# Kernel tuning notes

Measured on AMD Instinct MI355X. Metric: run time of the kernel, lower is better.

The kernel has to match this reference:

```python
import jax, jax.numpy as jnp
import numpy as np

N = 100000      # nodes
E = 1600000     # directed edges
F_IN = 9        # atom features (fixed by GCNConv(9, hidden))
H = 128         # hidden_channels
G = 64          # graphs in batch


def setup_inputs() -> dict:
    key = jax.random.key(0)
    ks = jax.random.split(key, 12)
    x = jax.random.normal(ks[0], (N, F_IN), dtype=jnp.float32)
    edge_index = jax.random.randint(ks[1], (2, E), 0, N, dtype=jnp.int64)
    batch = jnp.sort(jax.random.randint(ks[2], (N,), 0, G, dtype=jnp.int64))
    def lin_init(k, fan_in, fan_out):
        s = 1.0 / np.sqrt(fan_in)
        kw, kb = jax.random.split(k)
        W = jax.random.uniform(kw, (fan_in, fan_out), jnp.float32, -s, s)
        b = jax.random.uniform(kb, (fan_out,), jnp.float32, -s, s)
        return W, b
    W1, b1 = lin_init(ks[3], F_IN, H)
    W2, b2 = lin_init(ks[4], H, H)
    W3, b3 = lin_init(ks[5], H, H)
    lin_w, lin_b = lin_init(ks[6], H, 1)
    return {"x": x, "edge_index": edge_index, "batch": batch,
            "W1": W1, "b1": b1, "W2": W2, "b2": b2, "W3": W3, "b3": b3,
            "lin_w": lin_w, "lin_b": lin_b}


def reference(x, edge_index, batch, W1, b1, W2, b2, W3, b3, lin_w, lin_b):
    n = x.shape[0]
    # PyG GCNConv default: add self-loops, symmetric normalization D^-1/2 (A+I) D^-1/2
    loops = jnp.arange(n, dtype=edge_index.dtype)
    src = jnp.concatenate([edge_index[0], loops])   # [E+N]
    dst = jnp.concatenate([edge_index[1], loops])   # [E+N]
    deg = jax.ops.segment_sum(jnp.ones_like(dst, dtype=x.dtype), dst, num_segments=n)
    dinv = jnp.where(deg > 0, jax.lax.rsqrt(jnp.maximum(deg, 1e-12)), 0.0)
    norm = (dinv[src] * dinv[dst])[:, None]         # [E+N, 1]

    def gcn_conv(h, W, b):
        hw = h @ W                                   # [N, H]
        msg = hw[src] * norm                         # gather + scale  [E+N, H]
        return jax.ops.segment_sum(msg, dst, num_segments=n) + b  # scatter-add

    h = jax.nn.relu(gcn_conv(x, W1, b1))
    h = jax.nn.relu(gcn_conv(h, W2, b2))
    h = gcn_conv(h, W3, b3)

    # global_mean_pool over graph ids
    counts = jax.ops.segment_sum(jnp.ones((n,), x.dtype), batch, num_segments=G)
    pooled = jax.ops.segment_sum(h, batch, num_segments=G) / jnp.maximum(counts, 1.0)[:, None]
    return pooled @ lin_w + lin_b                    # [G, 1]
```

## Files before the change

kernel.cpp:

```cpp
#include <hip/hip_runtime.h>
#include <math.h>


#define CHUNK 2048

__device__ __forceinline__ int rankof(int i, int nq, int nr) {
  int c = i & 7;
  return c * nq + min(c, nr) + (i >> 3);
}
__device__ __forceinline__ unsigned short f2bf(float f) {
  unsigned int u = __float_as_uint(f);
  return (unsigned short)((u + 0x7fff + ((u >> 16) & 1)) >> 16);
}
__device__ __forceinline__ float bflo(unsigned int u) { return __uint_as_float(u << 16); }
__device__ __forceinline__ float bfhi(unsigned int u) { return __uint_as_float(u & 0xffff0000u); }


__global__ void deg_kernel(const int* __restrict__ dst, int* cnt_rank,
                           int E, int nq, int nr) {
  int e = blockIdx.x * blockDim.x + threadIdx.x;
  if (e < E) atomicAdd(&cnt_rank[rankof(dst[e], nq, nr)], 1);
}

__global__ void dinv_bsum_pad_kernel(const int* __restrict__ cnt_rank,
                                     float* __restrict__ dinv, int* bsum,
                                     const float* __restrict__ x,
                                     float* __restrict__ xp, int N, int nq, int nr) {
  __shared__ int s[256];
  int t = threadIdx.x;
  int gid = blockIdx.x * 256 + t;
  s[t] = (gid < N) ? cnt_rank[gid] : 0;
  if (gid < N) {
    int c = cnt_rank[rankof(gid, nq, nr)];
    float di = 1.0f / sqrtf((float)c + 1.0f);
    dinv[gid] = di;
    const float* xr = x + (size_t)gid * 9;
    float* xo = xp + (size_t)gid * 16;
    *(float4*)(xo + 0)  = make_float4(xr[0] * di, xr[1] * di, xr[2] * di, xr[3] * di);
    *(float4*)(xo + 4)  = make_float4(xr[4] * di, xr[5] * di, xr[6] * di, xr[7] * di);
    *(float4*)(xo + 8)  = make_float4(xr[8] * di, 0.0f, 0.0f, 0.0f);
    *(float4*)(xo + 12) = make_float4(0.0f, 0.0f, 0.0f, 0.0f);
  }
  __syncthreads();
  for (int off = 128; off > 0; off >>= 1) {
    if (t < off) s[t] += s[t + off];
    __syncthreads();
  }
  if (t == 0) bsum[blockIdx.x] = s[0];
}

__global__ void rowptr_vc0_kernel(const int* __restrict__ indeg, const int* __restrict__ bsum,
                                  int2* __restrict__ rows, int* cursor, int N, int E,
                                  int nq, int nr,
                                  const float* __restrict__ W3, const float* __restrict__ b3,
                                  const float* __restrict__ lin_w, const float* __restrict__ lin_b,
                                  float* v, float* c0) {
  __shared__ int ps[256];
  __shared__ int s[256];
  int t = threadIdx.x;
  int pref = 0;
  for (int q = t; q < blockIdx.x; q += 256) pref += bsum[q];
  ps[t] = pref;
  __syncthreads();
  for (int off = 128; off > 0; off >>= 1) {
    if (t < off) ps[t] += ps[t + off];
    __syncthreads();
  }
  int base = ps[0];
  int r = blockIdx.x * 256 + t;
  int val = (r < N) ? indeg[r] : 0;
  s[t] = val;
  __syncthreads();
  for (int off = 1; off < 256; off <<= 1) {
    int x = (t >= off) ? s[t - off] : 0;
    __syncthreads();
    s[t] += x;
    __syncthreads();
  }
  int excl = s[t] - val + base;
  if (r < N) {
    cursor[r] = excl;
    int c = 0;
#pragma unroll
    for (int cc = 1; cc < 8; ++cc) {
      int b = cc * nq + min(cc, nr);
      if (r >= b) c = cc;
    }
    int iinv = ((r - (c * nq + min(c, nr))) << 3) | c;
    rows[iinv] = make_int2(excl, excl + val);
  }
  if (blockIdx.x == 0) {
    if (t < 128) {
      float sv = 0.0f;
      for (int c = 0; c < 128; ++c) sv = fmaf(W3[t * 128 + c], lin_w[c], sv);
      v[t] = sv;
    } else if (t == 128) {
      float sv = 0.0f;
      for (int c = 0; c < 128; ++c) sv = fmaf(b3[c], lin_w[c], sv);
      c0[0] = sv + lin_b[0];
    }
  }
}

__global__ __launch_bounds__(256) void fill_part_kernel(const int* __restrict__ src,
                                                        const int* __restrict__ dst,
                                                        int* cursor, int* __restrict__ col,
                                                        int E, int nq, int nr) {
  int sub = blockIdx.x & 7;
  int base = (blockIdx.x >> 3) * CHUNK;
#pragma unroll
  for (int j = 0; j < CHUNK / 256; ++j) {
    int e = base + j * 256 + threadIdx.x;
    if (e < E) {
      int d = dst[e];
      if ((d & 7) == sub) {
        int p = atomicAdd(&cursor[rankof(d, nq, nr)], 1);
        col[p] = src[e];
      }
    }
  }
}


__global__ __launch_bounds__(256) void agg9_gemm1_kernel(const float* __restrict__ xp,
    const float* __restrict__ dinv, const int2* __restrict__ rows,
    const int* __restrict__ col, const float* __restrict__ W1,
    const float* __restrict__ b1, unsigned short* __restrict__ hA, int N) {
  __shared__ float sW[9 * 128];
  __shared__ float sx[256 * 9];
  __shared__ float sdi[256];
  int tid = threadIdx.x;
  for (int q = tid; q < 9 * 128; q += 256) sW[q] = W1[q];
  int i = blockIdx.x * 256 + tid;
  float4 A0, A1, A2, B0, B1, B2;
  A0 = A1 = A2 = B0 = B1 = B2 = make_float4(0.f, 0.f, 0.f, 0.f);
  float di = 0.0f;
  if (i < N) {
    di = dinv[i];
    const float4* xi = (const float4*)(xp + (size_t)i * 16);
    A0 = xi[0]; A1 = xi[1]; A2 = xi[2];
    int2 rw = rows[i];
    int rs = rw.x, re = rw.y;
    int e = rs;
    for (; e + 2 <= re; e += 2) {
      int c0 = __builtin_nontemporal_load(&col[e]);
      int c1 = __builtin_nontemporal_load(&col[e + 1]);
      const float4* q0 = (const float4*)(xp + (size_t)c0 * 16);
      const float4* q1 = (const float4*)(xp + (size_t)c1 * 16);
      float4 r0 = q0[0], r1 = q0[1], r2 = q0[2];
      float4 u0 = q1[0], u1 = q1[1], u2 = q1[2];
      A0.x += r0.x; A0.y += r0.y; A0.z += r0.z; A0.w += r0.w;
      A1.x += r1.x; A1.y += r1.y; A1.z += r1.z; A1.w += r1.w;
      A2.x += r2.x;
      B0.x += u0.x; B0.y += u0.y; B0.z += u0.z; B0.w += u0.w;
      B1.x += u1.x; B1.y += u1.y; B1.z += u1.z; B1.w += u1.w;
      B2.x += u2.x;
    }
    if (e < re) {
      int c0 = __builtin_nontemporal_load(&col[e]);
      const float4* q0 = (const float4*)(xp + (size_t)c0 * 16);
      float4 r0 = q0[0], r1 = q0[1], r2 = q0[2];
      A0.x += r0.x; A0.y += r0.y; A0.z += r0.z; A0.w += r0.w;
      A1.x += r1.x; A1.y += r1.y; A1.z += r1.z; A1.w += r1.w;
      A2.x += r2.x;
    }
  }
  sdi[tid] = di;
  float* so = sx + tid * 9;
  so[0] = (A0.x + B0.x) * di; so[1] = (A0.y + B0.y) * di; so[2] = (A0.z + B0.z) * di;
  so[3] = (A0.w + B0.w) * di; so[4] = (A1.x + B1.x) * di; so[5] = (A1.y + B1.y) * di;
  so[6] = (A1.z + B1.z) * di; so[7] = (A1.w + B1.w) * di; so[8] = (A2.x + B2.x) * di;
  __syncthreads();
  int c2 = tid & 63, rsub = tid >> 6;
  float wA[9], wB[9];
#pragma unroll
  for (int f = 0; f < 9; ++f) {
    wA[f] = sW[f * 128 + 2 * c2];
    wB[f] = sW[f * 128 + 2 * c2 + 1];
  }
  float biasA = b1[2 * c2], biasB = b1[2 * c2 + 1];
  int base = blockIdx.x * 256;
  for (int j = 0; j < 64; ++j) {
    int rl = j * 4 + rsub;
    int row = base + rl;
    if (row >= N) break;
    float sA = biasA, sB = biasB;
#pragma unroll
    for (int f = 0; f < 9; ++f) {
      float xv = sx[rl * 9 + f];
      sA = fmaf(xv, wA[f], sA);
      sB = fmaf(xv, wB[f], sB);
    }
    float d = sdi[rl];
    unsigned int pk = (unsigned int)f2bf(fmaxf(sA, 0.0f) * d)
                    | ((unsigned int)f2bf(fmaxf(sB, 0.0f) * d) << 16);
    *(unsigned int*)(hA + (size_t)row * 128 + 2 * c2) = pk;
  }
}


__global__ __launch_bounds__(256) void aggH_kernel(const unsigned short* __restrict__ h,
    const int2* __restrict__ rows, const int* __restrict__ col,
    float* __restrict__ g, int N) {
  int wave = threadIdx.x >> 6;
  int lane = threadIdx.x & 63;
  int half = lane >> 5;
  int l32  = lane & 31;
  int i = blockIdx.x * 4 + wave;
  if (i >= N) return;
  uint2 sp = *((const uint2*)(h + (size_t)i * 128) + l32);
  float m = half ? 0.0f : 1.0f;
  float4 a0 = make_float4(bflo(sp.x) * m, bfhi(sp.x) * m, bflo(sp.y) * m, bfhi(sp.y) * m);
  float4 a1 = make_float4(0.f, 0.f, 0.f, 0.f);
  float4 a2 = make_float4(0.f, 0.f, 0.f, 0.f);
  float4 a3 = make_float4(0.f, 0.f, 0.f, 0.f);
  int2 rw = rows[i];
  int rs = rw.x, re = rw.y;
  int e = rs;
  for (; e + 8 <= re; e += 8) {
    int c0 = __builtin_nontemporal_load(&col[e + half]);
    int c1 = __builtin_nontemporal_load(&col[e + 2 + half]);
    int c2 = __builtin_nontemporal_load(&col[e + 4 + half]);
    int c3 = __builtin_nontemporal_load(&col[e + 6 + half]);
    uint2 p0 = *((const uint2*)(h + (size_t)c0 * 128) + l32);
    uint2 p1 = *((const uint2*)(h + (size_t)c1 * 128) + l32);
    uint2 p2 = *((const uint2*)(h + (size_t)c2 * 128) + l32);
    uint2 p3 = *((const uint2*)(h + (size_t)c3 * 128) + l32);
    a0.x += bflo(p0.x); a0.y += bfhi(p0.x); a0.z += bflo(p0.y); a0.w += bfhi(p0.y);
    a1.x += bflo(p1.x); a1.y += bfhi(p1.x); a1.z += bflo(p1.y); a1.w += bfhi(p1.y);
    a2.x += bflo(p2.x); a2.y += bfhi(p2.x); a2.z += bflo(p2.y); a2.w += bfhi(p2.y);
    a3.x += bflo(p3.x); a3.y += bfhi(p3.x); a3.z += bflo(p3.y); a3.w += bfhi(p3.y);
  }
  if (e + 4 <= re) {
    int c0 = __builtin_nontemporal_load(&col[e + half]);
    int c1 = __builtin_nontemporal_load(&col[e + 2 + half]);
    uint2 p0 = *((const uint2*)(h + (size_t)c0 * 128) + l32);
    uint2 p1 = *((const uint2*)(h + (size_t)c1 * 128) + l32);
    a0.x += bflo(p0.x); a0.y += bfhi(p0.x); a0.z += bflo(p0.y); a0.w += bfhi(p0.y);
    a1.x += bflo(p1.x); a1.y += bfhi(p1.x); a1.z += bflo(p1.y); a1.w += bfhi(p1.y);
    e += 4;
  }
  if (e + 2 <= re) {
    int c0 = __builtin_nontemporal_load(&col[e + half]);
    uint2 p0 = *((const uint2*)(h + (size_t)c0 * 128) + l32);
    a2.x += bflo(p0.x); a2.y += bfhi(p0.x); a2.z += bflo(p0.y); a2.w += bfhi(p0.y);
    e += 2;
  }
  if (e < re) {
    int c0 = __builtin_nontemporal_load(&col[e]);
    uint2 p0 = *((const uint2*)(h + (size_t)c0 * 128) + l32);
    a3.x = fmaf(bflo(p0.x), 0.5f, a3.x); a3.y = fmaf(bfhi(p0.x), 0.5f, a3.y);
    a3.z = fmaf(bflo(p0.y), 0.5f, a3.z); a3.w = fmaf(bfhi(p0.y), 0.5f, a3.w);
  }
  float4 a = make_float4((a0.x + a1.x) + (a2.x + a3.x), (a0.y + a1.y) + (a2.y + a3.y),
                         (a0.z + a1.z) + (a2.z + a3.z), (a0.w + a1.w) + (a2.w + a3.w));
  a.x += __shfl_down(a.x, 32, 64);
  a.y += __shfl_down(a.y, 32, 64);
  a.z += __shfl_down(a.z, 32, 64);
  a.w += __shfl_down(a.w, 32, 64);
  if (half == 0) *((float4*)(g + (size_t)i * 128) + l32) = a;
}


__global__ __launch_bounds__(256, 4) void gemmz_kernel(const float* __restrict__ g,
    const float* __restrict__ W2, const float* __restrict__ dinv,
    const float* __restrict__ b2, const float* __restrict__ v,
    float* __restrict__ zd, int N) {
  __shared__ float Hs[32 * 132];
  __shared__ float Ws[32 * 128];
  int tid = threadIdx.x;
  int rb = blockIdx.x * 128;
  int tr = tid >> 4, tc = tid & 15;
  float acc[8][8];
#pragma unroll
  for (int r = 0; r < 8; ++r)
#pragma unroll
    for (int c = 0; c < 8; ++c) acc[r][c] = 0.0f;

  for (int kc = 0; kc < 128; kc += 32) {
#pragma unroll
    for (int j = 0; j < 4; ++j) {
      int q = tid + j * 256;
      int row = q >> 3;
      int kk = (q & 7) * 4;
      float4 vv = make_float4(0.f, 0.f, 0.f, 0.f);
      int grow = rb + row;
      if (grow < N) vv = *(const float4*)&g[(size_t)grow * 128 + kc + kk];
      Hs[(kk + 0) * 132 + row] = vv.x;
      Hs[(kk + 1) * 132 + row] = vv.y;
      Hs[(kk + 2) * 132 + row] = vv.z;
      Hs[(kk + 3) * 132 + row] = vv.w;
    }
#pragma unroll
    for (int j = 0; j < 4; ++j) {
      int q = tid + j * 256;
      int kr = q >> 5;
      int c4 = (q & 31) * 4;
      *(float4*)&Ws[kr * 128 + c4] = *(const float4*)&W2[(size_t)(kc + kr) * 128 + c4];
    }
    __syncthreads();
#pragma unroll 4
    for (int kk = 0; kk < 32; ++kk) {
      float4 h0 = *(const float4*)&Hs[kk * 132 + tr * 8];
      float4 h1 = *(const float4*)&Hs[kk * 132 + tr * 8 + 4];
      float4 w0 = *(const float4*)&Ws[kk * 128 + tc * 8];
      float4 w1 = *(const float4*)&Ws[kk * 128 + tc * 8 + 4];
      float av[8] = {h0.x, h0.y, h0.z, h0.w, h1.x, h1.y, h1.z, h1.w};
      float bv[8] = {w0.x, w0.y, w0.z, w0.w, w1.x, w1.y, w1.z, w1.w};
#pragma unroll
      for (int r = 0; r < 8; ++r)
#pragma unroll
        for (int c = 0; c < 8; ++c) acc[r][c] = fmaf(av[r], bv[c], acc[r][c]);
    }
    __syncthreads();
  }
  float4 ba = *((const float4*)b2 + tc * 2);
  float4 bb = *((const float4*)b2 + tc * 2 + 1);
  float4 va = *((const float4*)v + tc * 2);
  float4 vb = *((const float4*)v + tc * 2 + 1);
  float bc[8] = {ba.x, ba.y, ba.z, ba.w, bb.x, bb.y, bb.z, bb.w};
  float vc[8] = {va.x, va.y, va.z, va.w, vb.x, vb.y, vb.z, vb.w};
  float* red = Ws;
#pragma unroll
  for (int r = 0; r < 8; ++r) {
    int row = rb + tr * 8 + r;
    float p = 0.0f;
    if (row < N) {
      float dr = dinv[row];
#pragma unroll
      for (int c = 0; c < 8; ++c)
        p += fmaxf(fmaf(dr, acc[r][c], bc[c]), 0.0f) * vc[c];
    }
    red[(tr * 8 + r) * 17 + tc] = p;
  }
  __syncthreads();
  if (tid < 128) {
    int row = rb + tid;
    if (row < N) {
      float s = 0.0f;
#pragma unroll
      for (int j = 0; j < 16; ++j) s += red[tid * 17 + j];
      zd[row] = dinv[row] * s;
    }
  }
}


__global__ void agg1_pool_kernel(const float* __restrict__ zd, const float* __restrict__ dinv,
    const int2* __restrict__ rows, const int* __restrict__ col,
    const int* __restrict__ batch, float* gsum, float* gcnt, int N) {
  __shared__ float lsum[64];
  __shared__ float lcnt[64];
  int t = threadIdx.x;
  if (t < 64) { lsum[t] = 0.0f; lcnt[t] = 0.0f; }
  __syncthreads();
  int i = blockIdx.x * blockDim.x + t;
  if (i < N) {
    float acc = zd[i];
    int2 rw = rows[i];
    int rs = rw.x, re = rw.y;
    int e = rs;
    for (; e + 4 <= re; e += 4) {
      float z0 = zd[col[e]], z1 = zd[col[e + 1]];
      float z2 = zd[col[e + 2]], z3 = zd[col[e + 3]];
      acc += (z0 + z1) + (z2 + z3);
    }
    for (; e < re; ++e) acc += zd[col[e]];
    acc *= dinv[i];
    int gidx = batch[i];
    atomicAdd(&lsum[gidx], acc);
    atomicAdd(&lcnt[gidx], 1.0f);
  }
  __syncthreads();
  if (t < 64) {
    if (lsum[t] != 0.0f) atomicAdd(&gsum[t], lsum[t]);
    if (lcnt[t] != 0.0f) atomicAdd(&gcnt[t], lcnt[t]);
  }
}

__global__ void final_kernel(const float* __restrict__ gsum, const float* __restrict__ gcnt,
                             const float* __restrict__ c0, float* out, int G) {
  int g = threadIdx.x;
  if (g < G) out[g] = gsum[g] / fmaxf(gcnt[g], 1.0f) + c0[0];
}


extern "C" void kernel_launch(void* const* d_in, const int* in_sizes, int n_in,
                              void* d_out, int out_size, void* d_ws, size_t ws_size,
                              hipStream_t stream) {
  const float* x      = (const float*)d_in[0];
  const int*   eidx   = (const int*)d_in[1];
  const int*   batch  = (const int*)d_in[2];
  const float* W1     = (const float*)d_in[3];
  const float* b1     = (const float*)d_in[4];
  const float* W2     = (const float*)d_in[5];
  const float* b2     = (const float*)d_in[6];
  const float* W3     = (const float*)d_in[7];
  const float* b3     = (const float*)d_in[8];
  const float* lin_w  = (const float*)d_in[9];
  const float* lin_b  = (const float*)d_in[10];
  float* out = (float*)d_out;

  int N = in_sizes[0] / 9;
  int E = in_sizes[1] / 2;
  int G = out_size;
  const int* src = eidx;
  const int* dst = eidx + E;
  int nq = N >> 3, nr = N & 7;

  char* w = (char*)d_ws;
  size_t off = 0;
  auto alloc = [&](size_t bytes) -> void* {
    void* p = w + off;
    off += bytes;
    off = (off + 255) & ~(size_t)255;
    return p;
  };

  int nb = (N + 255) / 256;
  int nchunk = (E + CHUNK - 1) / CHUNK;
  int*   cursor = (int*)  alloc((size_t)N * 4);
  float* gsum   = (float*)alloc(64 * 4);
  float* gcnt   = (float*)alloc(64 * 4);
  size_t zspan = off;
  float* dinv   = (float*)alloc((size_t)N * 4);
  int2*  rows   = (int2*) alloc((size_t)N * 8);
  int*   bsum   = (int*)  alloc((size_t)nb * 4);
  int*   colsrc = (int*)  alloc((size_t)E * 4);
  unsigned short* hA = (unsigned short*)alloc((size_t)N * 128 * 2);
  float* g      = (float*)alloc((size_t)N * 128 * 4);
  float* zd     = (float*)alloc((size_t)N * 4);
  float* v      = (float*)alloc(128 * 4);
  float* c0     = (float*)alloc(4);
  float* xp     = g;

  hipMemsetAsync(d_ws, 0, zspan, stream);
  deg_kernel<<<(E + 255) / 256, 256, 0, stream>>>(dst, cursor, E, nq, nr);
  dinv_bsum_pad_kernel<<<nb, 256, 0, stream>>>(cursor, dinv, bsum, x, xp, N, nq, nr);
  rowptr_vc0_kernel<<<nb, 256, 0, stream>>>(cursor, bsum, rows, cursor, N, E, nq, nr,
                                            W3, b3, lin_w, lin_b, v, c0);
  fill_part_kernel<<<nchunk * 8, 256, 0, stream>>>(src, dst, cursor, colsrc, E, nq, nr);
  agg9_gemm1_kernel<<<nb, 256, 0, stream>>>(xp, dinv, rows, colsrc, W1, b1, hA, N);
  aggH_kernel<<<(N + 3) / 4, 256, 0, stream>>>(hA, rows, colsrc, g, N);
  gemmz_kernel<<<(N + 127) / 128, 256, 0, stream>>>(g, W2, dinv, b2, v, zd, N);
  agg1_pool_kernel<<<nb, 256, 0, stream>>>(zd, dinv, rows, colsrc, batch, gsum, gcnt, N);
  final_kernel<<<1, 64, 0, stream>>>(gsum, gcnt, c0, out, G);
}
```

Measured before the change: 409.8 us.

## Store aggregated hidden features in bf16 and widen aggH gathers to 16-byte loads

The layer-2 aggregation output g is now stored as packed bf16 instead of fp32, and the GEMM loader unpacks it. This halves the write traffic in aggH and the read traffic in gemmz. aggH also switches to 16-byte loads, with quarter-wave lanes covering four edges at a time, and uses a masked tail plus an xor-shuffle reduction. The first-layer aggregation loop is unrolled by 4. Rounding the aggregated features to bf16 adds some precision loss before the GEMM.

```diff
diff --git a/kernel.cpp b/kernel.cpp
--- a/kernel.cpp
+++ b/kernel.cpp
@@ -8,12 +8,22 @@
   int c = i & 7;
   return c * nq + min(c, nr) + (i >> 3);
 }
-__device__ __forceinline__ unsigned short f2bf(float f) {
+__device__ __forceinline__ unsigned int f2bf(float f) {
   unsigned int u = __float_as_uint(f);
-  return (unsigned short)((u + 0x7fff + ((u >> 16) & 1)) >> 16);
+  return ((u + 0x7fff + ((u >> 16) & 1)) >> 16);
 }
 __device__ __forceinline__ float bflo(unsigned int u) { return __uint_as_float(u << 16); }
 __device__ __forceinline__ float bfhi(unsigned int u) { return __uint_as_float(u & 0xffff0000u); }
+__device__ __forceinline__ void acc8(float4& p, float4& q, uint4 v) {
+  p.x += bflo(v.x); p.y += bfhi(v.x); p.z += bflo(v.y); p.w += bfhi(v.y);
+  q.x += bflo(v.z); q.y += bfhi(v.z); q.z += bflo(v.w); q.w += bfhi(v.w);
+}
+__device__ __forceinline__ void acc8w(float4& p, float4& q, uint4 v, float w) {
+  p.x = fmaf(bflo(v.x), w, p.x); p.y = fmaf(bfhi(v.x), w, p.y);
+  p.z = fmaf(bflo(v.y), w, p.z); p.w = fmaf(bfhi(v.y), w, p.w);
+  q.x = fmaf(bflo(v.z), w, q.x); q.y = fmaf(bfhi(v.z), w, q.y);
+  q.z = fmaf(bflo(v.w), w, q.z); q.w = fmaf(bfhi(v.w), w, q.w);
+}
 
 
 __global__ void deg_kernel(const int* __restrict__ dst, int* cnt_rank,
@@ -142,6 +152,32 @@
     int2 rw = rows[i];
     int rs = rw.x, re = rw.y;
     int e = rs;
+    for (; e + 4 <= re; e += 4) {
+      int c0 = __builtin_nontemporal_load(&col[e]);
+      int c1 = __builtin_nontemporal_load(&col[e + 1]);
+      int c2 = __builtin_nontemporal_load(&col[e + 2]);
+      int c3 = __builtin_nontemporal_load(&col[e + 3]);
+      const float4* q0 = (const float4*)(xp + (size_t)c0 * 16);
+      const float4* q1 = (const float4*)(xp + (size_t)c1 * 16);
+      const float4* q2 = (const float4*)(xp + (size_t)c2 * 16);
+      const float4* q3 = (const float4*)(xp + (size_t)c3 * 16);
+      float4 r0 = q0[0], r1 = q0[1], r2 = q0[2];
+      float4 u0 = q1[0], u1 = q1[1], u2 = q1[2];
+      float4 v0 = q2[0], v1 = q2[1], v2 = q2[2];
+      float4 w0 = q3[0], w1 = q3[1], w2 = q3[2];
+      A0.x += r0.x; A0.y += r0.y; A0.z += r0.z; A0.w += r0.w;
+      A1.x += r1.x; A1.y += r1.y; A1.z += r1.z; A1.w += r1.w;
+      A2.x += r2.x;
+      B0.x += u0.x; B0.y += u0.y; B0.z += u0.z; B0.w += u0.w;
+      B1.x += u1.x; B1.y += u1.y; B1.z += u1.z; B1.w += u1.w;
+      B2.x += u2.x;
+      A0.x += v0.x; A0.y += v0.y; A0.z += v0.z; A0.w += v0.w;
+      A1.x += v1.x; A1.y += v1.y; A1.z += v1.z; A1.w += v1.w;
+      A2.x += v2.x;
+      B0.x += w0.x; B0.y += w0.y; B0.z += w0.z; B0.w += w0.w;
+      B1.x += w1.x; B1.y += w1.y; B1.z += w1.z; B1.w += w1.w;
+      B2.x += w2.x;
+    }
     for (; e + 2 <= re; e += 2) {
       int c0 = __builtin_nontemporal_load(&col[e]);
       int c1 = __builtin_nontemporal_load(&col[e + 1]);
@@ -171,14 +207,14 @@
   so[3] = (A0.w + B0.w) * di; so[4] = (A1.x + B1.x) * di; so[5] = (A1.y + B1.y) * di;
   so[6] = (A1.z + B1.z) * di; so[7] = (A1.w + B1.w) * di; so[8] = (A2.x + B2.x) * di;
   __syncthreads();
-  int c2 = tid & 63, rsub = tid >> 6;
+  int c2i = tid & 63, rsub = tid >> 6;
   float wA[9], wB[9];
 #pragma unroll
   for (int f = 0; f < 9; ++f) {
-    wA[f] = sW[f * 128 + 2 * c2];
-    wB[f] = sW[f * 128 + 2 * c2 + 1];
-  }
-  float biasA = b1[2 * c2], biasB = b1[2 * c2 + 1];
+    wA[f] = sW[f * 128 + 2 * c2i];
+    wB[f] = sW[f * 128 + 2 * c2i + 1];
+  }
+  float biasA = b1[2 * c2i], biasB = b1[2 * c2i + 1];
   int base = blockIdx.x * 256;
   for (int j = 0; j < 64; ++j) {
     int rl = j * 4 + rsub;
@@ -192,77 +228,75 @@
       sB = fmaf(xv, wB[f], sB);
     }
     float d = sdi[rl];
-    unsigned int pk = (unsigned int)f2bf(fmaxf(sA, 0.0f) * d)
-                    | ((unsigned int)f2bf(fmaxf(sB, 0.0f) * d) << 16);
-    *(unsigned int*)(hA + (size_t)row * 128 + 2 * c2) = pk;
+    unsigned int pk = f2bf(fmaxf(sA, 0.0f) * d) | (f2bf(fmaxf(sB, 0.0f) * d) << 16);
+    *(unsigned int*)(hA + (size_t)row * 128 + 2 * c2i) = pk;
   }
 }
 
 
 __global__ __launch_bounds__(256) void aggH_kernel(const unsigned short* __restrict__ h,
     const int2* __restrict__ rows, const int* __restrict__ col,
-    float* __restrict__ g, int N) {
+    unsigned short* __restrict__ g, int N) {
   int wave = threadIdx.x >> 6;
   int lane = threadIdx.x & 63;
-  int half = lane >> 5;
-  int l32  = lane & 31;
+  int q4 = lane >> 4;
+  int l16 = lane & 15;
   int i = blockIdx.x * 4 + wave;
   if (i >= N) return;
-  uint2 sp = *((const uint2*)(h + (size_t)i * 128) + l32);
-  float m = half ? 0.0f : 1.0f;
-  float4 a0 = make_float4(bflo(sp.x) * m, bfhi(sp.x) * m, bflo(sp.y) * m, bfhi(sp.y) * m);
-  float4 a1 = make_float4(0.f, 0.f, 0.f, 0.f);
-  float4 a2 = make_float4(0.f, 0.f, 0.f, 0.f);
-  float4 a3 = make_float4(0.f, 0.f, 0.f, 0.f);
+  uint4 sp = *((const uint4*)(h + (size_t)i * 128) + l16);
+  float m = (q4 == 0) ? 1.0f : 0.0f;
+  float4 A0 = make_float4(0.f, 0.f, 0.f, 0.f), A1 = A0, B0 = A0, B1 = A0;
+  float4 C0 = A0, C1 = A0, D0 = A0, D1 = A0;
+  acc8w(A0, A1, sp, m);
   int2 rw = rows[i];
   int rs = rw.x, re = rw.y;
   int e = rs;
-  for (; e + 8 <= re; e += 8) {
-    int c0 = __builtin_nontemporal_load(&col[e + half]);
-    int c1 = __builtin_nontemporal_load(&col[e + 2 + half]);
-    int c2 = __builtin_nontemporal_load(&col[e + 4 + half]);
-    int c3 = __builtin_nontemporal_load(&col[e + 6 + half]);
-    uint2 p0 = *((const uint2*)(h + (size_t)c0 * 128) + l32);
-    uint2 p1 = *((const uint2*)(h + (size_t)c1 * 128) + l32);
-    uint2 p2 = *((const uint2*)(h + (size_t)c2 * 128) + l32);
-    uint2 p3 = *((const uint2*)(h + (size_t)c3 * 128) + l32);
-    a0.x += bflo(p0.x); a0.y += bfhi(p0.x); a0.z += bflo(p0.y); a0.w += bfhi(p0.y);
-    a1.x += bflo(p1.x); a1.y += bfhi(p1.x); a1.z += bflo(p1.y); a1.w += bfhi(p1.y);
-    a2.x += bflo(p2.x); a2.y += bfhi(p2.x); a2.z += bflo(p2.y); a2.w += bfhi(p2.y);
-    a3.x += bflo(p3.x); a3.y += bfhi(p3.x); a3.z += bflo(p3.y); a3.w += bfhi(p3.y);
-  }
-  if (e + 4 <= re) {
-    int c0 = __builtin_nontemporal_load(&col[e + half]);
-    int c1 = __builtin_nontemporal_load(&col[e + 2 + half]);
-    uint2 p0 = *((const uint2*)(h + (size_t)c0 * 128) + l32);
-    uint2 p1 = *((const uint2*)(h + (size_t)c1 * 128) + l32);
-    a0.x += bflo(p0.x); a0.y += bfhi(p0.x); a0.z += bflo(p0.y); a0.w += bfhi(p0.y);
-    a1.x += bflo(p1.x); a1.y += bfhi(p1.x); a1.z += bflo(p1.y); a1.w += bfhi(p1.y);
-    e += 4;
-  }
-  if (e + 2 <= re) {
-    int c0 = __builtin_nontemporal_load(&col[e + half]);
-    uint2 p0 = *((const uint2*)(h + (size_t)c0 * 128) + l32);
-    a2.x += bflo(p0.x); a2.y += bfhi(p0.x); a2.z += bflo(p0.y); a2.w += bfhi(p0.y);
-    e += 2;
+  for (; e + 16 <= re; e += 16) {
+    int c0 = __builtin_nontemporal_load(&col[e + q4]);
+    int c1 = __builtin_nontemporal_load(&col[e + 4 + q4]);
+    int c2 = __builtin_nontemporal_load(&col[e + 8 + q4]);
+    int c3 = __builtin_nontemporal_load(&col[e + 12 + q4]);
+    uint4 p0 = *((const uint4*)(h + (size_t)c0 * 128) + l16);
+    uint4 p1 = *((const uint4*)(h + (size_t)c1 * 128) + l16);
+    uint4 p2 = *((const uint4*)(h + (size_t)c2 * 128) + l16);
+    uint4 p3 = *((const uint4*)(h + (size_t)c3 * 128) + l16);
+    acc8(A0, A1, p0); acc8(B0, B1, p1); acc8(C0, C1, p2); acc8(D0, D1, p3);
+  }
+  for (; e + 4 <= re; e += 4) {
+    int c0 = __builtin_nontemporal_load(&col[e + q4]);
+    uint4 p0 = *((const uint4*)(h + (size_t)c0 * 128) + l16);
+    acc8(C0, C1, p0);
   }
   if (e < re) {
-    int c0 = __builtin_nontemporal_load(&col[e]);
-    uint2 p0 = *((const uint2*)(h + (size_t)c0 * 128) + l32);
-    a3.x = fmaf(bflo(p0.x), 0.5f, a3.x); a3.y = fmaf(bfhi(p0.x), 0.5f, a3.y);
-    a3.z = fmaf(bflo(p0.y), 0.5f, a3.z); a3.w = fmaf(bfhi(p0.y), 0.5f, a3.w);
-  }
-  float4 a = make_float4((a0.x + a1.x) + (a2.x + a3.x), (a0.y + a1.y) + (a2.y + a3.y),
-                         (a0.z + a1.z) + (a2.z + a3.z), (a0.w + a1.w) + (a2.w + a3.w));
-  a.x += __shfl_down(a.x, 32, 64);
-  a.y += __shfl_down(a.y, 32, 64);
-  a.z += __shfl_down(a.z, 32, 64);
-  a.w += __shfl_down(a.w, 32, 64);
-  if (half == 0) *((float4*)(g + (size_t)i * 128) + l32) = a;
-}
-
-
-__global__ __launch_bounds__(256, 4) void gemmz_kernel(const float* __restrict__ g,
+    int idx = e + q4;
+    int c0 = __builtin_nontemporal_load(&col[min(idx, re - 1)]);
+    uint4 p0 = *((const uint4*)(h + (size_t)c0 * 128) + l16);
+    float w = (idx < re) ? 1.0f : 0.0f;
+    acc8w(D0, D1, p0, w);
+  }
+  float4 s0 = make_float4((A0.x + B0.x) + (C0.x + D0.x), (A0.y + B0.y) + (C0.y + D0.y),
+                          (A0.z + B0.z) + (C0.z + D0.z), (A0.w + B0.w) + (C0.w + D0.w));
+  float4 s1 = make_float4((A1.x + B1.x) + (C1.x + D1.x), (A1.y + B1.y) + (C1.y + D1.y),
+                          (A1.z + B1.z) + (C1.z + D1.z), (A1.w + B1.w) + (C1.w + D1.w));
+#pragma unroll
+  for (int mk = 16; mk <= 32; mk <<= 1) {
+    s0.x += __shfl_xor(s0.x, mk, 64); s0.y += __shfl_xor(s0.y, mk, 64);
+    s0.z += __shfl_xor(s0.z, mk, 64); s0.w += __shfl_xor(s0.w, mk, 64);
+    s1.x += __shfl_xor(s1.x, mk, 64); s1.y += __shfl_xor(s1.y, mk, 64);
+    s1.z += __shfl_xor(s1.z, mk, 64); s1.w += __shfl_xor(s1.w, mk, 64);
+  }
+  if (q4 == 0) {
+    uint4 o;
+    o.x = f2bf(s0.x) | (f2bf(s0.y) << 16);
+    o.y = f2bf(s0.z) | (f2bf(s0.w) << 16);
+    o.z = f2bf(s1.x) | (f2bf(s1.y) << 16);
+    o.w = f2bf(s1.z) | (f2bf(s1.w) << 16);
+    *((uint4*)(g + (size_t)i * 128) + l16) = o;
+  }
+}
+
+
+__global__ __launch_bounds__(256, 4) void gemmz_kernel(const unsigned short* __restrict__ g,
     const float* __restrict__ W2, const float* __restrict__ dinv,
     const float* __restrict__ b2, const float* __restrict__ v,
     float* __restrict__ zd, int N) {
@@ -279,17 +313,18 @@
 
   for (int kc = 0; kc < 128; kc += 32) {
 #pragma unroll
-    for (int j = 0; j < 4; ++j) {
+    for (int j = 0; j < 2; ++j) {
       int q = tid + j * 256;
-      int row = q >> 3;
-      int kk = (q & 7) * 4;
-      float4 vv = make_float4(0.f, 0.f, 0.f, 0.f);
+      int row = q >> 2;
+      int seg = q & 3;
+      uint4 vv = make_uint4(0u, 0u, 0u, 0u);
       int grow = rb + row;
-      if (grow < N) vv = *(const float4*)&g[(size_t)grow * 128 + kc + kk];
-      Hs[(kk + 0) * 132 + row] = vv.x;
-      Hs[(kk + 1) * 132 + row] = vv.y;
-      Hs[(kk + 2) * 132 + row] = vv.z;
-      Hs[(kk + 3) * 132 + row] = vv.w;
+      if (grow < N) vv = *((const uint4*)(g + (size_t)grow * 128 + kc) + seg);
+      int kk = seg * 8;
+      Hs[(kk + 0) * 132 + row] = bflo(vv.x); Hs[(kk + 1) * 132 + row] = bfhi(vv.x);
+      Hs[(kk + 2) * 132 + row] = bflo(vv.y); Hs[(kk + 3) * 132 + row] = bfhi(vv.y);
+      Hs[(kk + 4) * 132 + row] = bflo(vv.z); Hs[(kk + 5) * 132 + row] = bfhi(vv.z);
+      Hs[(kk + 6) * 132 + row] = bflo(vv.w); Hs[(kk + 7) * 132 + row] = bfhi(vv.w);
     }
 #pragma unroll
     for (int j = 0; j < 4; ++j) {
@@ -428,11 +463,11 @@
   int*   bsum   = (int*)  alloc((size_t)nb * 4);
   int*   colsrc = (int*)  alloc((size_t)E * 4);
   unsigned short* hA = (unsigned short*)alloc((size_t)N * 128 * 2);
-  float* g      = (float*)alloc((size_t)N * 128 * 4);
+  unsigned short* g  = (unsigned short*)alloc((size_t)N * 128 * 2);
   float* zd     = (float*)alloc((size_t)N * 4);
   float* v      = (float*)alloc(128 * 4);
   float* c0     = (float*)alloc(4);
-  float* xp     = g;
+  float* xp     = (float*)g;
 
   hipMemsetAsync(d_ws, 0, zspan, stream);
   deg_kernel<<<(E + 255) / 256, 256, 0, stream>>>(dst, cursor, E, nq, nr);
```

New measurement: 413.0 us. About the same (+0.8%).

## Store aggregated layer-2 features as bf16 and unroll layer-1 gather by four

Applied to the files above, without the earlier changes.

The intermediate buffer g written by the aggregation kernel and read by the GEMM kernel changes from fp32 to bf16, halving its write and read traffic. The GEMM load path now reads eight bf16 values per 16-byte load and expands them into shared memory. The first-layer neighbour gather is also unrolled to four edges per iteration for more loads in flight. The bf16 rounding of g adds numerical error, and xp now aliases a smaller buffer (N*256 bytes, which still fits the N*64 padded x).

```diff
diff --git a/kernel.cpp b/kernel.cpp
--- a/kernel.cpp
+++ b/kernel.cpp
@@ -8,9 +8,9 @@
   int c = i & 7;
   return c * nq + min(c, nr) + (i >> 3);
 }
-__device__ __forceinline__ unsigned short f2bf(float f) {
+__device__ __forceinline__ unsigned int f2bf(float f) {
   unsigned int u = __float_as_uint(f);
-  return (unsigned short)((u + 0x7fff + ((u >> 16) & 1)) >> 16);
+  return ((u + 0x7fff + ((u >> 16) & 1)) >> 16);
 }
 __device__ __forceinline__ float bflo(unsigned int u) { return __uint_as_float(u << 16); }
 __device__ __forceinline__ float bfhi(unsigned int u) { return __uint_as_float(u & 0xffff0000u); }
@@ -142,6 +142,32 @@
     int2 rw = rows[i];
     int rs = rw.x, re = rw.y;
     int e = rs;
+    for (; e + 4 <= re; e += 4) {
+      int c0 = __builtin_nontemporal_load(&col[e]);
+      int c1 = __builtin_nontemporal_load(&col[e + 1]);
+      int c2 = __builtin_nontemporal_load(&col[e + 2]);
+      int c3 = __builtin_nontemporal_load(&col[e + 3]);
+      const float4* q0 = (const float4*)(xp + (size_t)c0 * 16);
+      const float4* q1 = (const float4*)(xp + (size_t)c1 * 16);
+      const float4* q2 = (const float4*)(xp + (size_t)c2 * 16);
+      const float4* q3 = (const float4*)(xp + (size_t)c3 * 16);
+      float4 r0 = q0[0], r1 = q0[1], r2 = q0[2];
+      float4 u0 = q1[0], u1 = q1[1], u2 = q1[2];
+      float4 v0 = q2[0], v1 = q2[1], v2 = q2[2];
+      float4 w0 = q3[0], w1 = q3[1], w2 = q3[2];
+      A0.x += r0.x; A0.y += r0.y; A0.z += r0.z; A0.w += r0.w;
+      A1.x += r1.x; A1.y += r1.y; A1.z += r1.z; A1.w += r1.w;
+      A2.x += r2.x;
+      B0.x += u0.x; B0.y += u0.y; B0.z += u0.z; B0.w += u0.w;
+      B1.x += u1.x; B1.y += u1.y; B1.z += u1.z; B1.w += u1.w;
+      B2.x += u2.x;
+      A0.x += v0.x; A0.y += v0.y; A0.z += v0.z; A0.w += v0.w;
+      A1.x += v1.x; A1.y += v1.y; A1.z += v1.z; A1.w += v1.w;
+      A2.x += v2.x;
+      B0.x += w0.x; B0.y += w0.y; B0.z += w0.z; B0.w += w0.w;
+      B1.x += w1.x; B1.y += w1.y; B1.z += w1.z; B1.w += w1.w;
+      B2.x += w2.x;
+    }
     for (; e + 2 <= re; e += 2) {
       int c0 = __builtin_nontemporal_load(&col[e]);
       int c1 = __builtin_nontemporal_load(&col[e + 1]);
@@ -171,14 +197,14 @@
   so[3] = (A0.w + B0.w) * di; so[4] = (A1.x + B1.x) * di; so[5] = (A1.y + B1.y) * di;
   so[6] = (A1.z + B1.z) * di; so[7] = (A1.w + B1.w) * di; so[8] = (A2.x + B2.x) * di;
   __syncthreads();
-  int c2 = tid & 63, rsub = tid >> 6;
+  int c2i = tid & 63, rsub = tid >> 6;
   float wA[9], wB[9];
 #pragma unroll
   for (int f = 0; f < 9; ++f) {
-    wA[f] = sW[f * 128 + 2 * c2];
-    wB[f] = sW[f * 128 + 2 * c2 + 1];
-  }
-  float biasA = b1[2 * c2], biasB = b1[2 * c2 + 1];
+    wA[f] = sW[f * 128 + 2 * c2i];
+    wB[f] = sW[f * 128 + 2 * c2i + 1];
+  }
+  float biasA = b1[2 * c2i], biasB = b1[2 * c2i + 1];
   int base = blockIdx.x * 256;
   for (int j = 0; j < 64; ++j) {
     int rl = j * 4 + rsub;
@@ -192,16 +218,15 @@
       sB = fmaf(xv, wB[f], sB);
     }
     float d = sdi[rl];
-    unsigned int pk = (unsigned int)f2bf(fmaxf(sA, 0.0f) * d)
-                    | ((unsigned int)f2bf(fmaxf(sB, 0.0f) * d) << 16);
-    *(unsigned int*)(hA + (size_t)row * 128 + 2 * c2) = pk;
+    unsigned int pk = f2bf(fmaxf(sA, 0.0f) * d) | (f2bf(fmaxf(sB, 0.0f) * d) << 16);
+    *(unsigned int*)(hA + (size_t)row * 128 + 2 * c2i) = pk;
   }
 }
 
 
 __global__ __launch_bounds__(256) void aggH_kernel(const unsigned short* __restrict__ h,
     const int2* __restrict__ rows, const int* __restrict__ col,
-    float* __restrict__ g, int N) {
+    unsigned short* __restrict__ g, int N) {
   int wave = threadIdx.x >> 6;
   int lane = threadIdx.x & 63;
   int half = lane >> 5;
@@ -258,11 +283,16 @@
   a.y += __shfl_down(a.y, 32, 64);
   a.z += __shfl_down(a.z, 32, 64);
   a.w += __shfl_down(a.w, 32, 64);
-  if (half == 0) *((float4*)(g + (size_t)i * 128) + l32) = a;
-}
-
-
-__global__ __launch_bounds__(256, 4) void gemmz_kernel(const float* __restrict__ g,
+  if (half == 0) {
+    uint2 o;
+    o.x = f2bf(a.x) | (f2bf(a.y) << 16);
+    o.y = f2bf(a.z) | (f2bf(a.w) << 16);
+    *((uint2*)(g + (size_t)i * 128) + l32) = o;
+  }
+}
+
+
+__global__ __launch_bounds__(256, 4) void gemmz_kernel(const unsigned short* __restrict__ g,
     const float* __restrict__ W2, const float* __restrict__ dinv,
     const float* __restrict__ b2, const float* __restrict__ v,
     float* __restrict__ zd, int N) {
@@ -279,17 +309,18 @@
 
   for (int kc = 0; kc < 128; kc += 32) {
 #pragma unroll
-    for (int j = 0; j < 4; ++j) {
+    for (int j = 0; j < 2; ++j) {
       int q = tid + j * 256;
-      int row = q >> 3;
-      int kk = (q & 7) * 4;
-      float4 vv = make_float4(0.f, 0.f, 0.f, 0.f);
+      int row = q >> 2;
+      int seg = q & 3;
+      uint4 vv = make_uint4(0u, 0u, 0u, 0u);
       int grow = rb + row;
-      if (grow < N) vv = *(const float4*)&g[(size_t)grow * 128 + kc + kk];
-      Hs[(kk + 0) * 132 + row] = vv.x;
-      Hs[(kk + 1) * 132 + row] = vv.y;
-      Hs[(kk + 2) * 132 + row] = vv.z;
-      Hs[(kk + 3) * 132 + row] = vv.w;
+      if (grow < N) vv = *((const uint4*)(g + (size_t)grow * 128 + kc) + seg);
+      int kk = seg * 8;
+      Hs[(kk + 0) * 132 + row] = bflo(vv.x); Hs[(kk + 1) * 132 + row] = bfhi(vv.x);
+      Hs[(kk + 2) * 132 + row] = bflo(vv.y); Hs[(kk + 3) * 132 + row] = bfhi(vv.y);
+      Hs[(kk + 4) * 132 + row] = bflo(vv.z); Hs[(kk + 5) * 132 + row] = bfhi(vv.z);
+      Hs[(kk + 6) * 132 + row] = bflo(vv.w); Hs[(kk + 7) * 132 + row] = bfhi(vv.w);
     }
 #pragma unroll
     for (int j = 0; j < 4; ++j) {
@@ -428,11 +459,11 @@
   int*   bsum   = (int*)  alloc((size_t)nb * 4);
   int*   colsrc = (int*)  alloc((size_t)E * 4);
   unsigned short* hA = (unsigned short*)alloc((size_t)N * 128 * 2);
-  float* g      = (float*)alloc((size_t)N * 128 * 4);
+  unsigned short* g  = (unsigned short*)alloc((size_t)N * 128 * 2);
   float* zd     = (float*)alloc((size_t)N * 4);
   float* v      = (float*)alloc(128 * 4);
   float* c0     = (float*)alloc(4);
-  float* xp     = g;
+  float* xp     = (float*)g;
 
   hipMemsetAsync(d_ws, 0, zspan, stream);
   deg_kernel<<<(E + 255) / 256, 256, 0, stream>>>(dst, cursor, E, nq, nr);
```

New measurement: 405.6 us. About the same (-1.0%).

## Use bf16 MFMA for layer-2 GEMM and store aggregates in bf16

Applied to the files above, without the earlier changes.

The fp32 register-tiled layer-2 GEMM is replaced by a bf16 MFMA (16x16x32) kernel that reads a W2 matrix pre-packed into fragment order inside the rowptr kernel. The aggregated hidden buffer g is now stored in bf16, halving its write and read traffic. The padded input features xp are also stored in bf16 for the first aggregation gather. This trades precision on the intermediate activations for lower memory traffic and matrix-core throughput, and adds a zeroed pad row so out-of-range tile rows can be read safely.

```diff
diff --git a/kernel.cpp b/kernel.cpp
--- a/kernel.cpp
+++ b/kernel.cpp
@@ -3,14 +3,17 @@
 
 
 #define CHUNK 2048
+
+using short8 = __attribute__((ext_vector_type(8))) short;
+using floatx4 = __attribute__((ext_vector_type(4))) float;
 
 __device__ __forceinline__ int rankof(int i, int nq, int nr) {
   int c = i & 7;
   return c * nq + min(c, nr) + (i >> 3);
 }
-__device__ __forceinline__ unsigned short f2bf(float f) {
+__device__ __forceinline__ unsigned int f2bf(float f) {
   unsigned int u = __float_as_uint(f);
-  return (unsigned short)((u + 0x7fff + ((u >> 16) & 1)) >> 16);
+  return ((u + 0x7fff + ((u >> 16) & 1)) >> 16);
 }
 __device__ __forceinline__ float bflo(unsigned int u) { return __uint_as_float(u << 16); }
 __device__ __forceinline__ float bfhi(unsigned int u) { return __uint_as_float(u & 0xffff0000u); }
@@ -25,7 +28,7 @@
 __global__ void dinv_bsum_pad_kernel(const int* __restrict__ cnt_rank,
                                      float* __restrict__ dinv, int* bsum,
                                      const float* __restrict__ x,
-                                     float* __restrict__ xp, int N, int nq, int nr) {
+                                     unsigned short* __restrict__ xp, int N, int nq, int nr) {
   __shared__ int s[256];
   int t = threadIdx.x;
   int gid = blockIdx.x * 256 + t;
@@ -35,11 +38,14 @@
     float di = 1.0f / sqrtf((float)c + 1.0f);
     dinv[gid] = di;
     const float* xr = x + (size_t)gid * 9;
-    float* xo = xp + (size_t)gid * 16;
-    *(float4*)(xo + 0)  = make_float4(xr[0] * di, xr[1] * di, xr[2] * di, xr[3] * di);
-    *(float4*)(xo + 4)  = make_float4(xr[4] * di, xr[5] * di, xr[6] * di, xr[7] * di);
-    *(float4*)(xo + 8)  = make_float4(xr[8] * di, 0.0f, 0.0f, 0.0f);
-    *(float4*)(xo + 12) = make_float4(0.0f, 0.0f, 0.0f, 0.0f);
+    unsigned int w0 = f2bf(xr[0] * di) | (f2bf(xr[1] * di) << 16);
+    unsigned int w1 = f2bf(xr[2] * di) | (f2bf(xr[3] * di) << 16);
+    unsigned int w2 = f2bf(xr[4] * di) | (f2bf(xr[5] * di) << 16);
+    unsigned int w3 = f2bf(xr[6] * di) | (f2bf(xr[7] * di) << 16);
+    unsigned int w4 = f2bf(xr[8] * di);
+    uint4* xo = (uint4*)(xp + (size_t)gid * 16);
+    xo[0] = make_uint4(w0, w1, w2, w3);
+    xo[1] = make_uint4(w4, 0u, 0u, 0u);
   }
   __syncthreads();
   for (int off = 128; off > 0; off >>= 1) {
@@ -54,6 +60,8 @@
                                   int nq, int nr,
                                   const float* __restrict__ W3, const float* __restrict__ b3,
                                   const float* __restrict__ lin_w, const float* __restrict__ lin_b,
+                                  const float* __restrict__ W2, unsigned short* __restrict__ W2p,
+                                  unsigned short* __restrict__ g,
                                   float* v, float* c0) {
   __shared__ int ps[256];
   __shared__ int s[256];
@@ -90,6 +98,7 @@
     rows[iinv] = make_int2(excl, excl + val);
   }
   if (blockIdx.x == 0) {
+    if (t < 64) ((unsigned int*)g)[(size_t)N * 64 + t] = 0u;
     if (t < 128) {
       float sv = 0.0f;
       for (int c = 0; c < 128; ++c) sv = fmaf(W3[t * 128 + c], lin_w[c], sv);
@@ -99,6 +108,18 @@
       for (int c = 0; c < 128; ++c) sv = fmaf(b3[c], lin_w[c], sv);
       c0[0] = sv + lin_b[0];
     }
+  } else if (blockIdx.x <= 8) {
+    int ntile = blockIdx.x - 1;
+    int kstep = t >> 6, lane = t & 63;
+    int n = ntile * 16 + (lane & 15);
+    int k0 = kstep * 32 + ((lane >> 4) & 3) * 8;
+    unsigned int pk[4];
+#pragma unroll
+    for (int jj = 0; jj < 4; ++jj)
+      pk[jj] = f2bf(W2[(size_t)(k0 + 2 * jj) * 128 + n])
+             | (f2bf(W2[(size_t)(k0 + 2 * jj + 1) * 128 + n]) << 16);
+    *(uint4*)(W2p + (size_t)(((ntile * 4 + kstep) * 64 + lane) * 8)) =
+        make_uint4(pk[0], pk[1], pk[2], pk[3]);
   }
 }
 
@@ -122,7 +143,7 @@
 }
 
 
-__global__ __launch_bounds__(256) void agg9_gemm1_kernel(const float* __restrict__ xp,
+__global__ __launch_bounds__(256) void agg9_gemm1_kernel(const unsigned short* __restrict__ xp,
     const float* __restrict__ dinv, const int2* __restrict__ rows,
     const int* __restrict__ col, const float* __restrict__ W1,
     const float* __restrict__ b1, unsigned short* __restrict__ hA, int N) {
@@ -132,53 +153,60 @@
   int tid = threadIdx.x;
   for (int q = tid; q < 9 * 128; q += 256) sW[q] = W1[q];
   int i = blockIdx.x * 256 + tid;
-  float4 A0, A1, A2, B0, B1, B2;
-  A0 = A1 = A2 = B0 = B1 = B2 = make_float4(0.f, 0.f, 0.f, 0.f);
+  float A[9], B[9];
+#pragma unroll
+  for (int f = 0; f < 9; ++f) { A[f] = 0.0f; B[f] = 0.0f; }
   float di = 0.0f;
   if (i < N) {
     di = dinv[i];
-    const float4* xi = (const float4*)(xp + (size_t)i * 16);
-    A0 = xi[0]; A1 = xi[1]; A2 = xi[2];
+    const unsigned short* xi = xp + (size_t)i * 16;
+    uint4 s0 = *(const uint4*)xi;
+    unsigned int s1 = *(const unsigned int*)(xi + 8);
+    A[0] = bflo(s0.x); A[1] = bfhi(s0.x); A[2] = bflo(s0.y); A[3] = bfhi(s0.y);
+    A[4] = bflo(s0.z); A[5] = bfhi(s0.z); A[6] = bflo(s0.w); A[7] = bfhi(s0.w);
+    A[8] = bflo(s1);
     int2 rw = rows[i];
     int rs = rw.x, re = rw.y;
     int e = rs;
     for (; e + 2 <= re; e += 2) {
       int c0 = __builtin_nontemporal_load(&col[e]);
       int c1 = __builtin_nontemporal_load(&col[e + 1]);
-      const float4* q0 = (const float4*)(xp + (size_t)c0 * 16);
-      const float4* q1 = (const float4*)(xp + (size_t)c1 * 16);
-      float4 r0 = q0[0], r1 = q0[1], r2 = q0[2];
-      float4 u0 = q1[0], u1 = q1[1], u2 = q1[2];
-      A0.x += r0.x; A0.y += r0.y; A0.z += r0.z; A0.w += r0.w;
-      A1.x += r1.x; A1.y += r1.y; A1.z += r1.z; A1.w += r1.w;
-      A2.x += r2.x;
-      B0.x += u0.x; B0.y += u0.y; B0.z += u0.z; B0.w += u0.w;
-      B1.x += u1.x; B1.y += u1.y; B1.z += u1.z; B1.w += u1.w;
-      B2.x += u2.x;
+      const unsigned short* p0 = xp + (size_t)c0 * 16;
+      const unsigned short* p1 = xp + (size_t)c1 * 16;
+      uint4 q0 = *(const uint4*)p0;
+      unsigned int t0 = *(const unsigned int*)(p0 + 8);
+      uint4 q1 = *(const uint4*)p1;
+      unsigned int t1 = *(const unsigned int*)(p1 + 8);
+      A[0] += bflo(q0.x); A[1] += bfhi(q0.x); A[2] += bflo(q0.y); A[3] += bfhi(q0.y);
+      A[4] += bflo(q0.z); A[5] += bfhi(q0.z); A[6] += bflo(q0.w); A[7] += bfhi(q0.w);
+      A[8] += bflo(t0);
+      B[0] += bflo(q1.x); B[1] += bfhi(q1.x); B[2] += bflo(q1.y); B[3] += bfhi(q1.y);
+      B[4] += bflo(q1.z); B[5] += bfhi(q1.z); B[6] += bflo(q1.w); B[7] += bfhi(q1.w);
+      B[8] += bflo(t1);
     }
     if (e < re) {
       int c0 = __builtin_nontemporal_load(&col[e]);
-      const float4* q0 = (const float4*)(xp + (size_t)c0 * 16);
-      float4 r0 = q0[0], r1 = q0[1], r2 = q0[2];
-      A0.x += r0.x; A0.y += r0.y; A0.z += r0.z; A0.w += r0.w;
-      A1.x += r1.x; A1.y += r1.y; A1.z += r1.z; A1.w += r1.w;
-      A2.x += r2.x;
+      const unsigned short* p0 = xp + (size_t)c0 * 16;
+      uint4 q0 = *(const uint4*)p0;
+      unsigned int t0 = *(const unsigned int*)(p0 + 8);
+      A[0] += bflo(q0.x); A[1] += bfhi(q0.x); A[2] += bflo(q0.y); A[3] += bfhi(q0.y);
+      A[4] += bflo(q0.z); A[5] += bfhi(q0.z); A[6] += bflo(q0.w); A[7] += bfhi(q0.w);
+      A[8] += bflo(t0);
     }
   }
   sdi[tid] = di;
   float* so = sx + tid * 9;
-  so[0] = (A0.x + B0.x) * di; so[1] = (A0.y + B0.y) * di; so[2] = (A0.z + B0.z) * di;
-  so[3] = (A0.w + B0.w) * di; so[4] = (A1.x + B1.x) * di; so[5] = (A1.y + B1.y) * di;
-  so[6] = (A1.z + B1.z) * di; so[7] = (A1.w + B1.w) * di; so[8] = (A2.x + B2.x) * di;
-  __syncthreads();
-  int c2 = tid & 63, rsub = tid >> 6;
+#pragma unroll
+  for (int f = 0; f < 9; ++f) so[f] = (A[f] + B[f]) * di;
+  __syncthreads();
+  int c2i = tid & 63, rsub = tid >> 6;
   float wA[9], wB[9];
 #pragma unroll
   for (int f = 0; f < 9; ++f) {
-    wA[f] = sW[f * 128 + 2 * c2];
-    wB[f] = sW[f * 128 + 2 * c2 + 1];
-  }
-  float biasA = b1[2 * c2], biasB = b1[2 * c2 + 1];
+    wA[f] = sW[f * 128 + 2 * c2i];
+    wB[f] = sW[f * 128 + 2 * c2i + 1];
+  }
+  float biasA = b1[2 * c2i], biasB = b1[2 * c2i + 1];
   int base = blockIdx.x * 256;
   for (int j = 0; j < 64; ++j) {
     int rl = j * 4 + rsub;
@@ -192,16 +220,15 @@
       sB = fmaf(xv, wB[f], sB);
     }
     float d = sdi[rl];
-    unsigned int pk = (unsigned int)f2bf(fmaxf(sA, 0.0f) * d)
-                    | ((unsigned int)f2bf(fmaxf(sB, 0.0f) * d) << 16);
-    *(unsigned int*)(hA + (size_t)row * 128 + 2 * c2) = pk;
+    unsigned int pk = f2bf(fmaxf(sA, 0.0f) * d) | (f2bf(fmaxf(sB, 0.0f) * d) << 16);
+    *(unsigned int*)(hA + (size_t)row * 128 + 2 * c2i) = pk;
   }
 }
 
 
 __global__ __launch_bounds__(256) void aggH_kernel(const unsigned short* __restrict__ h,
     const int2* __restrict__ rows, const int* __restrict__ col,
-    float* __restrict__ g, int N) {
+    unsigned short* __restrict__ g, int N) {
   int wave = threadIdx.x >> 6;
   int lane = threadIdx.x & 63;
   int half = lane >> 5;
@@ -258,90 +285,54 @@
   a.y += __shfl_down(a.y, 32, 64);
   a.z += __shfl_down(a.z, 32, 64);
   a.w += __shfl_down(a.w, 32, 64);
-  if (half == 0) *((float4*)(g + (size_t)i * 128) + l32) = a;
-}
-
-
-__global__ __launch_bounds__(256, 4) void gemmz_kernel(const float* __restrict__ g,
-    const float* __restrict__ W2, const float* __restrict__ dinv,
+  if (half == 0) {
+    uint2 o;
+    o.x = f2bf(a.x) | (f2bf(a.y) << 16);
+    o.y = f2bf(a.z) | (f2bf(a.w) << 16);
+    *((uint2*)(g + (size_t)i * 128) + l32) = o;
+  }
+}
+
+
+__global__ __launch_bounds__(256) void gemmz_kernel(const unsigned short* __restrict__ g,
+    const unsigned short* __restrict__ W2p, const float* __restrict__ dinv,
     const float* __restrict__ b2, const float* __restrict__ v,
     float* __restrict__ zd, int N) {
-  __shared__ float Hs[32 * 132];
-  __shared__ float Ws[32 * 128];
-  int tid = threadIdx.x;
-  int rb = blockIdx.x * 128;
-  int tr = tid >> 4, tc = tid & 15;
-  float acc[8][8];
-#pragma unroll
-  for (int r = 0; r < 8; ++r)
-#pragma unroll
-    for (int c = 0; c < 8; ++c) acc[r][c] = 0.0f;
-
-  for (int kc = 0; kc < 128; kc += 32) {
-#pragma unroll
-    for (int j = 0; j < 4; ++j) {
-      int q = tid + j * 256;
-      int row = q >> 3;
-      int kk = (q & 7) * 4;
-      float4 vv = make_float4(0.f, 0.f, 0.f, 0.f);
-      int grow = rb + row;
-      if (grow < N) vv = *(const float4*)&g[(size_t)grow * 128 + kc + kk];
-      Hs[(kk + 0) * 132 + row] = vv.x;
-      Hs[(kk + 1) * 132 + row] = vv.y;
-      Hs[(kk + 2) * 132 + row] = vv.z;
-      Hs[(kk + 3) * 132 + row] = vv.w;
-    }
-#pragma unroll
-    for (int j = 0; j < 4; ++j) {
-      int q = tid + j * 256;
-      int kr = q >> 5;
-      int c4 = (q & 31) * 4;
-      *(float4*)&Ws[kr * 128 + c4] = *(const float4*)&W2[(size_t)(kc + kr) * 128 + c4];
-    }
-    __syncthreads();
-#pragma unroll 4
-    for (int kk = 0; kk < 32; ++kk) {
-      float4 h0 = *(const float4*)&Hs[kk * 132 + tr * 8];
-      float4 h1 = *(const float4*)&Hs[kk * 132 + tr * 8 + 4];
-      float4 w0 = *(const float4*)&Ws[kk * 128 + tc * 8];
-      float4 w1 = *(const float4*)&Ws[kk * 128 + tc * 8 + 4];
-      float av[8] = {h0.x, h0.y, h0.z, h0.w, h1.x, h1.y, h1.z, h1.w};
-      float bv[8] = {w0.x, w0.y, w0.z, w0.w, w1.x, w1.y, w1.z, w1.w};
-#pragma unroll
-      for (int r = 0; r < 8; ++r)
-#pragma unroll
-        for (int c = 0; c < 8; ++c) acc[r][c] = fmaf(av[r], bv[c], acc[r][c]);
-    }
-    __syncthreads();
-  }
-  float4 ba = *((const float4*)b2 + tc * 2);
-  float4 bb = *((const float4*)b2 + tc * 2 + 1);
-  float4 va = *((const float4*)v + tc * 2);
-  float4 vb = *((const float4*)v + tc * 2 + 1);
-  float bc[8] = {ba.x, ba.y, ba.z, ba.w, bb.x, bb.y, bb.z, bb.w};
-  float vc[8] = {va.x, va.y, va.z, va.w, vb.x, vb.y, vb.z, vb.w};
-  float* red = Ws;
-#pragma unroll
-  for (int r = 0; r < 8; ++r) {
-    int row = rb + tr * 8 + r;
+  int wave = threadIdx.x >> 6, lane = threadIdx.x & 63;
+  int rb16 = blockIdx.x * 64 + wave * 16;
+  int m = lane & 15, quad = lane >> 4;
+  int rowA = rb16 + m;
+  const unsigned short* gp = g + (size_t)((rowA < N) ? rowA : N) * 128 + quad * 8;
+  floatx4 acc[8];
+#pragma unroll
+  for (int t = 0; t < 8; ++t) acc[t] = (floatx4){0.f, 0.f, 0.f, 0.f};
+#pragma unroll
+  for (int ks = 0; ks < 4; ++ks) {
+    short8 afrag = *(const short8*)(gp + ks * 32);
+#pragma unroll
+    for (int t = 0; t < 8; ++t) {
+      short8 bfrag = *(const short8*)(W2p + (size_t)(((t * 4 + ks) * 64 + lane) * 8));
+      acc[t] = __builtin_amdgcn_mfma_f32_16x16x32_bf16(afrag, bfrag, acc[t], 0, 0, 0);
+    }
+  }
+  float b2c[8], vc[8];
+#pragma unroll
+  for (int t = 0; t < 8; ++t) {
+    int ncol = t * 16 + m;
+    b2c[t] = b2[ncol];
+    vc[t] = v[ncol];
+  }
+#pragma unroll
+  for (int reg = 0; reg < 4; ++reg) {
+    int grow = rb16 + quad * 4 + reg;
+    float dr = (grow < N) ? dinv[grow] : 0.0f;
     float p = 0.0f;
-    if (row < N) {
-      float dr = dinv[row];
-#pragma unroll
-      for (int c = 0; c < 8; ++c)
-        p += fmaxf(fmaf(dr, acc[r][c], bc[c]), 0.0f) * vc[c];
-    }
-    red[(tr * 8 + r) * 17 + tc] = p;
-  }
-  __syncthreads();
-  if (tid < 128) {
-    int row = rb + tid;
-    if (row < N) {
-      float s = 0.0f;
-#pragma unroll
-      for (int j = 0; j < 16; ++j) s += red[tid * 17 + j];
-      zd[row] = dinv[row] * s;
-    }
+#pragma unroll
+    for (int t = 0; t < 8; ++t)
+      p += fmaxf(fmaf(dr, acc[t][reg], b2c[t]), 0.0f) * vc[t];
+#pragma unroll
+    for (int mk = 1; mk <= 8; mk <<= 1) p += __shfl_xor(p, mk, 64);
+    if (m == 0 && grow < N) zd[grow] = dr * p;
   }
 }
 
@@ -427,22 +418,23 @@
   int2*  rows   = (int2*) alloc((size_t)N * 8);
   int*   bsum   = (int*)  alloc((size_t)nb * 4);
   int*   colsrc = (int*)  alloc((size_t)E * 4);
-  unsigned short* hA = (unsigned short*)alloc((size_t)N * 128 * 2);
-  float* g      = (float*)alloc((size_t)N * 128 * 4);
+  unsigned short* hA  = (unsigned short*)alloc((size_t)N * 128 * 2);
+  unsigned short* g   = (unsigned short*)alloc((size_t)(N + 1) * 128 * 2);
+  unsigned short* W2p = (unsigned short*)alloc(8 * 4 * 64 * 8 * 2);
   float* zd     = (float*)alloc((size_t)N * 4);
   float* v      = (float*)alloc(128 * 4);
   float* c0     = (float*)alloc(4);
-  float* xp     = g;
+  unsigned short* xp = g;
 
   hipMemsetAsync(d_ws, 0, zspan, stream);
   deg_kernel<<<(E + 255) / 256, 256, 0, stream>>>(dst, cursor, E, nq, nr);
   dinv_bsum_pad_kernel<<<nb, 256, 0, stream>>>(cursor, dinv, bsum, x, xp, N, nq, nr);
   rowptr_vc0_kernel<<<nb, 256, 0, stream>>>(cursor, bsum, rows, cursor, N, E, nq, nr,
-                                            W3, b3, lin_w, lin_b, v, c0);
+                                            W3, b3, lin_w, lin_b, W2, W2p, g, v, c0);
   fill_part_kernel<<<nchunk * 8, 256, 0, stream>>>(src, dst, cursor, colsrc, E, nq, nr);
   agg9_gemm1_kernel<<<nb, 256, 0, stream>>>(xp, dinv, rows, colsrc, W1, b1, hA, N);
   aggH_kernel<<<(N + 3) / 4, 256, 0, stream>>>(hA, rows, colsrc, g, N);
-  gemmz_kernel<<<(N + 127) / 128, 256, 0, stream>>>(g, W2, dinv, b2, v, zd, N);
+  gemmz_kernel<<<(N + 63) / 64, 256, 0, stream>>>(g, W2p, dinv, b2, v, zd, N);
   agg1_pool_kernel<<<nb, 256, 0, stream>>>(zd, dinv, rows, colsrc, batch, gsum, gcnt, N);
   final_kernel<<<1, 64, 0, stream>>>(gsum, gcnt, c0, out, G);
 }
```

Measured after the change: 368.0 us. 1.11x faster.
